# Kernel optimization log

Measured on AMD Instinct MI355X. Metric: run time of the kernel, lower is better.

## Reference

```python
import jax, jax.numpy as jnp
import numpy as np

F_, H_, W_ = 8, 24, 24          # video_shape
KS, DIL = 3, 1                  # kernel_size, dilation (cubic)
HEADS, DH, DIM = 8, 64, 512
N_TOK = F_ * H_ * W_            # 4608 video tokens (+1 BOS)
PAD = DIL * (KS - 1) // 2
SCALE = DH ** -0.5


def _geometry():
    """Precompute im2col gather indices into the padded volume and the causal mask."""
    fp, hp, wp = F_ + 2 * PAD, H_ + 2 * PAD, W_ + 2 * PAD
    tg, ig, jg = np.meshgrid(np.arange(F_), np.arange(H_), np.arange(W_), indexing='ij')
    a = np.arange(KS) * DIL
    at, ai, aj = np.meshgrid(a, a, a, indexing='ij')  # window offsets
    # query (t,i,j) in original coords == window start in padded coords
    tc = tg.reshape(-1, 1) + at.reshape(1, -1)  # [N, K3]
    ic = ig.reshape(-1, 1) + ai.reshape(1, -1)
    jc = jg.reshape(-1, 1) + aj.reshape(1, -1)
    idx = (tc * hp + ic) * wp + jc              # flat index into padded volume
    # token-id volume padded with sentinel N_TOK (matches F.pad value=max_num_tokens)
    tok = np.full((fp, hp, wp), N_TOK, dtype=np.int64)
    tok[PAD:PAD + F_, PAD:PAD + H_, PAD:PAD + W_] = np.arange(N_TOK).reshape(F_, H_, W_)
    unfolded = tok.reshape(-1)[idx]             # [N, K3]
    causal = np.arange(N_TOK)[:, None] < unfolded  # True = masked (padding is N_TOK > all)
    mask = np.concatenate([np.zeros((N_TOK, 1), bool), causal], axis=1)  # BOS never masked
    return idx, mask

_IDX_NP, _MASK_NP = _geometry()


def setup_inputs() -> dict:
    key = jax.random.key(0)
    ks = jax.random.split(key, 6)
    n = N_TOK + 1
    return {
        'x': jax.random.normal(ks[0], (1, n, DIM), jnp.float32),
        'w_q': jax.random.normal(ks[1], (DIM, HEADS * DH), jnp.float32) * 0.02,
        'w_kv': jax.random.normal(ks[2], (DIM, 2 * HEADS * DH), jnp.float32) * 0.02,
        'w_talk': jax.random.normal(ks[3], (HEADS, HEADS), jnp.float32) * 0.1,
        'w_out': jax.random.normal(ks[4], (HEADS * DH, DIM), jnp.float32) * 0.02,
        'b_out': jnp.zeros((DIM,), jnp.float32),
    }


def reference(x, w_q, w_kv, w_talk, w_out, b_out):
    idx = jnp.asarray(_IDX_NP)
    mask = jnp.asarray(_MASK_NP)
    b, n, _ = x.shape
    bh = b * HEADS
    fp, hp, wp = F_ + 2 * PAD, H_ + 2 * PAD, W_ + 2 * PAD

    q = x @ w_q                                  # [b, n, h*d]
    k, v = jnp.split(x @ w_kv, 2, axis=-1)

    def to_heads(t):
        return t.reshape(b, n, HEADS, DH).transpose(0, 2, 1, 3).reshape(bh, n, DH)

    q, k, v = map(to_heads, (q, k, v))
    q = q[:, 1:] * SCALE                         # drop BOS query
    k_bos, v_bos = k[:, :1], v[:, :1]            # [bh, 1, d]
    k, v = k[:, 1:], v[:, 1:]

    def pad_unfold(t):
        vol = t.reshape(bh, F_, H_, W_, DH)
        vol = jnp.pad(vol, ((0, 0), (PAD, PAD), (PAD, PAD), (PAD, PAD), (0, 0)))
        flat = vol.reshape(bh, fp * hp * wp, DH)
        return flat[:, idx]                      # [bh, N, K3, d]

    k_unf, v_unf = pad_unfold(k), pad_unfold(v)
    k_full = jnp.concatenate([jnp.broadcast_to(k_bos[:, None], (bh, N_TOK, 1, DH)), k_unf], axis=2)
    v_full = jnp.concatenate([jnp.broadcast_to(v_bos[:, None], (bh, N_TOK, 1, DH)), v_unf], axis=2)

    sim = jnp.einsum('bid,bijd->bij', q, k_full)           # [bh, N, 1+K3]
    sim = jnp.where(mask[None], -jnp.finfo(sim.dtype).max, sim)
    attn = jax.nn.softmax(sim, axis=-1)
    attn = attn.reshape(b, HEADS, N_TOK, -1)
    attn = jnp.einsum('gh,bhij->bgij', w_talk, attn)       # talking heads (1x1 conv)
    attn = attn.reshape(bh, N_TOK, -1)

    out = jnp.einsum('bij,bijd->bid', attn, v_full)        # [bh, N, d]
    out = jnp.concatenate([v_bos, out], axis=1)            # BOS output = v_bos
    out = out.reshape(b, HEADS, n, DH).transpose(0, 2, 1, 3).reshape(b, n, HEADS * DH)
    return out @ w_out + b_out
```

## Files before the change

### kernel.cpp

```cpp
#include <hip/hip_runtime.h>
#include <cfloat>
#include <cmath>

#define F_   8
#define H_   24
#define W_   24
#define NTOK 4608
#define NSEQ 4609
#define MPAD 4736
#define DIM  512
#define QKVC 1536
#define NNB  28
#define SCALEF 0.125f

typedef unsigned short ushort_t;
typedef __attribute__((ext_vector_type(8))) short short8v;
typedef __attribute__((ext_vector_type(8))) unsigned short ushort8v;
typedef __attribute__((ext_vector_type(4))) unsigned short ushort4v;
typedef __attribute__((ext_vector_type(4))) float floatx4;

typedef const __attribute__((address_space(1))) unsigned int guint_t;
typedef __attribute__((address_space(3))) unsigned int luint_t;

__device__ __forceinline__ float bf2f(unsigned short u) {
    return __uint_as_float(((unsigned)u) << 16);
}
__device__ __forceinline__ unsigned short f2bf(float f) {
    unsigned u = __float_as_uint(f);
    unsigned r = (u + 0x7FFFu + ((u >> 16) & 1u)) >> 16;
    return (unsigned short)r;
}

#define XBLK 1184
#define CONV_BLOCKS (XBLK + 192 + 64)

__global__ __launch_bounds__(256) void conv_k(
    const float* __restrict__ x, const float* __restrict__ wq,
    const float* __restrict__ wkv, const float* __restrict__ wout,
    ushort_t* __restrict__ xb, ushort_t* __restrict__ wcatT,
    ushort_t* __restrict__ woutT)
{
    const int bid = blockIdx.x, tid = threadIdx.x;
    __shared__ ushort_t tile[64][72];

    if (bid < XBLK) {
        int e0 = (bid * 256 + tid) * 8;
        int row = e0 >> 9;
        float4 a = make_float4(0.f, 0.f, 0.f, 0.f);
        float4 b = make_float4(0.f, 0.f, 0.f, 0.f);
        if (row < NSEQ) {
            a = *reinterpret_cast<const float4*>(&x[e0]);
            b = *reinterpret_cast<const float4*>(&x[e0 + 4]);
        }
        ushort8v o;
        o[0] = f2bf(a.x); o[1] = f2bf(a.y); o[2] = f2bf(a.z); o[3] = f2bf(a.w);
        o[4] = f2bf(b.x); o[5] = f2bf(b.y); o[6] = f2bf(b.z); o[7] = f2bf(b.w);
        *reinterpret_cast<ushort8v*>(&xb[e0]) = o;
        return;
    }

    int blk2 = bid - XBLK;
    const float* src; int ld, cb; ushort_t* dst; int k0;
    if (blk2 < 192) {
        int nt = blk2 >> 3, kt = blk2 & 7;
        int n0 = nt * 64;
        if (n0 < 512) { src = wq;  ld = 512;  cb = n0; }
        else          { src = wkv; ld = 1024; cb = n0 - 512; }
        dst = wcatT + (size_t)n0 * 512;
        k0 = kt * 64;
    } else {
        int b3 = blk2 - 192;
        int nt = b3 >> 3, kt = b3 & 7;
        src = wout; ld = 512; cb = nt * 64;
        dst = woutT + (size_t)(nt * 64) * 512;
        k0 = kt * 64;
    }

    {
        int r = tid >> 4, c4 = (tid & 15) * 4;
        #pragma unroll
        for (int p = 0; p < 4; ++p) {
            int rr = r + p * 16;
            float4 v = *reinterpret_cast<const float4*>(&src[(size_t)(k0 + rr) * ld + cb + c4]);
            tile[c4 + 0][rr] = f2bf(v.x);
            tile[c4 + 1][rr] = f2bf(v.y);
            tile[c4 + 2][rr] = f2bf(v.z);
            tile[c4 + 3][rr] = f2bf(v.w);
        }
    }
    __syncthreads();
    {
        int nl = tid >> 3, ks = (tid & 7) * 8;
        #pragma unroll
        for (int rep = 0; rep < 2; ++rep) {
            int nn = nl + rep * 32;
            ushort8v vv = *reinterpret_cast<const ushort8v*>(&tile[nn][ks]);
            *reinterpret_cast<ushort8v*>(&dst[(size_t)nn * 512 + k0 + ks]) = vv;
        }
    }
}

template<int BM, bool F32OUT>
__global__ __launch_bounds__(256, 3) void gemm_k(
    const ushort_t* __restrict__ A,
    const ushort_t* __restrict__ BT,
    const float* __restrict__ bias,
    void* __restrict__ Cv, int ldc)
{
    __shared__ ushort_t sA[BM * 64];
    __shared__ ushort_t sB[128 * 64];
    const int tid = threadIdx.x;

    const int nwg = gridDim.x * gridDim.y;
    const int orig = blockIdx.y * gridDim.x + blockIdx.x;
    const int xcd = orig & 7;
    const int qq = nwg >> 3, rr8 = nwg & 7;
    const int wg = (xcd < rr8 ? xcd * (qq + 1) : rr8 * (qq + 1) + (xcd - rr8) * qq)
                   + (orig >> 3);
    const int row0 = (wg / gridDim.x) * BM;
    const int col0 = (wg % gridDim.x) * 128;

    const int wid = tid >> 6, lane = tid & 63;
    const int wr = wid >> 1, wc = wid & 1;
    const int l15 = lane & 15, kp = lane >> 4;
    constexpr int MR = BM / 32;

    floatx4 acc[MR][4];
    #pragma unroll
    for (int m = 0; m < MR; ++m)
        #pragma unroll
        for (int n = 0; n < 4; ++n)
            acc[m][n] = (floatx4){0.f, 0.f, 0.f, 0.f};

    const ushort_t* Abase = A + (size_t)row0 * 512;
    const ushort_t* Bbase = BT + (size_t)col0 * 512;

    for (int kt = 0; kt < 8; ++kt) {
        const int k0 = kt * 64;
        #pragma unroll
        for (int rnd = 0; rnd < BM / 32; ++rnd) {
            int r = rnd * 32 + (tid >> 3);
            int gs = (tid & 7) ^ (r & 7);
            __builtin_amdgcn_global_load_lds(
                (guint_t*)(Abase + (size_t)r * 512 + k0 + gs * 8),
                (luint_t*)(sA + r * 64 + (tid & 7) * 8), 16, 0, 0);
        }
        #pragma unroll
        for (int rnd = 0; rnd < 4; ++rnd) {
            int r = rnd * 32 + (tid >> 3);
            int gs = (tid & 7) ^ (r & 7);
            __builtin_amdgcn_global_load_lds(
                (guint_t*)(Bbase + (size_t)r * 512 + k0 + gs * 8),
                (luint_t*)(sB + r * 64 + (tid & 7) * 8), 16, 0, 0);
        }
        __syncthreads();

        #pragma unroll
        for (int kk = 0; kk < 2; ++kk) {
            short8v af[MR], bfr[4];
            #pragma unroll
            for (int m = 0; m < MR; ++m) {
                int r = wr * (BM / 2) + m * 16 + l15;
                int slot = kk * 4 + kp;
                af[m] = *(const short8v*)&sA[r * 64 + ((slot ^ (r & 7)) << 3)];
            }
            #pragma unroll
            for (int n = 0; n < 4; ++n) {
                int r = wc * 64 + n * 16 + l15;
                int slot = kk * 4 + kp;
                bfr[n] = *(const short8v*)&sB[r * 64 + ((slot ^ (r & 7)) << 3)];
            }
            #pragma unroll
            for (int m = 0; m < MR; ++m)
                #pragma unroll
                for (int n = 0; n < 4; ++n)
                    acc[m][n] = __builtin_amdgcn_mfma_f32_16x16x32_bf16(
                        af[m], bfr[n], acc[m][n], 0, 0, 0);
        }
        __syncthreads();
    }

    if (!F32OUT) {
        ushort_t* C = (ushort_t*)Cv;
        #pragma unroll
        for (int m = 0; m < MR; ++m) {
            int rb = row0 + wr * (BM / 2) + m * 16 + kp * 4;
            #pragma unroll
            for (int n = 0; n < 4; ++n) {
                int col = col0 + wc * 64 + n * 16 + l15;
                #pragma unroll
                for (int q = 0; q < 4; ++q)
                    C[(size_t)(rb + q) * ldc + col] = f2bf(acc[m][n][q]);
            }
        }
    } else {
        float* C = (float*)Cv;
        #pragma unroll
        for (int m = 0; m < MR; ++m) {
            int rb = row0 + wr * (BM / 2) + m * 16 + kp * 4;
            #pragma unroll
            for (int n = 0; n < 4; ++n) {
                int col = col0 + wc * 64 + n * 16 + l15;
                float bv = bias[col];
                #pragma unroll
                for (int q = 0; q < 4; ++q)
                    if (rb + q < NSEQ)
                        C[(size_t)(rb + q) * ldc + col] = acc[m][n][q] + bv;
            }
        }
    }
}

__global__ __launch_bounds__(256) void attn_k(
    const ushort_t* __restrict__ qkv,
    const float* __restrict__ wtalk,
    ushort_t* __restrict__ outh)
{
    const int lane = threadIdx.x & 63;
    const int i = blockIdx.x * 4 + (threadIdx.x >> 6);
    const int h = lane >> 3, s = lane & 7;

    const int t = i / (H_ * W_), rem = i % (H_ * W_);
    const int yy = rem / W_, xx = rem % W_;

    int rowj = -1;
    if (lane == 0) rowj = 0;
    else if (lane < NNB) {
        int e = lane - 1;
        int dt = e / 9 - 1, dy = (e / 3) % 3 - 1, dx = e % 3 - 1;
        int nt = t + dt, ny = yy + dy, nx = xx + dx;
        bool valid = ((unsigned)nt < (unsigned)F_) && ((unsigned)ny < (unsigned)H_) &&
                     ((unsigned)nx < (unsigned)W_);
        int u = (nt * H_ + ny) * W_ + nx;
        rowj = (valid && u <= i) ? (u + 1) : -1;
    }

    int rows[NNB];
    #pragma unroll
    for (int j = 0; j < NNB; ++j) rows[j] = __shfl(rowj, j, 64);

    float qf[8];
    {
        ushort8v qv = *(const ushort8v*)&qkv[(size_t)(i + 1) * QKVC + lane * 8];
        #pragma unroll
        for (int e = 0; e < 8; ++e) qf[e] = bf2f(qv[e]);
    }

    float ps[NNB];
    #pragma unroll
    for (int j = 0; j < NNB; ++j) {
        int r = rows[j] < 0 ? 0 : rows[j];
        ushort8v kv = *(const ushort8v*)&qkv[(size_t)r * QKVC + 512 + lane * 8];
        float a = 0.f;
        #pragma unroll
        for (int e = 0; e < 8; ++e) a += qf[e] * bf2f(kv[e]);
        ps[j] = a;
    }

    float v1[14];
    {
        bool hi = (s & 1) != 0;
        #pragma unroll
        for (int m = 0; m < 14; ++m) {
            float keep = hi ? ps[2 * m + 1] : ps[2 * m];
            float oth  = hi ? ps[2 * m]     : ps[2 * m + 1];
            v1[m] = keep + __shfl_xor(oth, 1, 64);
        }
    }
    float v2[8];
    {
        bool hi = (s & 2) != 0;
        #pragma unroll
        for (int m = 0; m < 7; ++m) {
            float keep = hi ? v1[2 * m + 1] : v1[2 * m];
            float oth  = hi ? v1[2 * m]     : v1[2 * m + 1];
            v2[m] = keep + __shfl_xor(oth, 2, 64);
        }
        v2[7] = 0.f;
    }
    float simk[4];
    {
        bool hi = (s & 4) != 0;
        #pragma unroll
        for (int k = 0; k < 4; ++k) {
            float keep = hi ? v2[2 * k + 1] : v2[2 * k];
            float oth  = hi ? v2[2 * k]     : v2[2 * k + 1];
            simk[k] = keep + __shfl_xor(oth, 4, 64);
        }
    }
    #pragma unroll
    for (int k = 0; k < 4; ++k) {
        int j = s + 8 * k;
        int rj = __shfl(rowj, j, 64);
        simk[k] = (rj >= 0) ? simk[k] * SCALEF : -FLT_MAX;
    }

    float mx = fmaxf(fmaxf(simk[0], simk[1]), fmaxf(simk[2], simk[3]));
    mx = fmaxf(mx, __shfl_xor(mx, 1, 64));
    mx = fmaxf(mx, __shfl_xor(mx, 2, 64));
    mx = fmaxf(mx, __shfl_xor(mx, 4, 64));
    float att[4];
    float S = 0.f;
    #pragma unroll
    for (int k = 0; k < 4; ++k) { att[k] = __expf(simk[k] - mx); S += att[k]; }
    S += __shfl_xor(S, 1, 64);
    S += __shfl_xor(S, 2, 64);
    S += __shfl_xor(S, 4, 64);
    float inv = 1.f / S;
    #pragma unroll
    for (int k = 0; k < 4; ++k) att[k] *= inv;

    float wtg[8];
    #pragma unroll
    for (int hh = 0; hh < 8; ++hh) wtg[hh] = wtalk[h * 8 + hh];
    float pk[4];
    #pragma unroll
    for (int k = 0; k < 4; ++k) {
        float acc = 0.f;
        #pragma unroll
        for (int hh = 0; hh < 8; ++hh)
            acc += wtg[hh] * __shfl(att[k], hh * 8 + s, 64);
        pk[k] = acc;
    }

    float o[8];
    #pragma unroll
    for (int e = 0; e < 8; ++e) o[e] = 0.f;
    #pragma unroll
    for (int j = 0; j < NNB; ++j) {
        float pj = __shfl(pk[j >> 3], h * 8 + (j & 7), 64);
        int r = rows[j] < 0 ? 0 : rows[j];
        ushort8v vv = *(const ushort8v*)&qkv[(size_t)r * QKVC + 1024 + lane * 8];
        #pragma unroll
        for (int e = 0; e < 8; ++e) o[e] += pj * bf2f(vv[e]);
    }

    ushort8v ov;
    #pragma unroll
    for (int e = 0; e < 8; ++e) ov[e] = f2bf(o[e]);
    *(ushort8v*)&outh[(size_t)(i + 1) * DIM + lane * 8] = ov;

    if (i == 0) {
        ushort8v bv = *(const ushort8v*)&qkv[1024 + lane * 8];
        *(ushort8v*)&outh[lane * 8] = bv;
    }
}

extern "C" void kernel_launch(void* const* d_in, const int* in_sizes, int n_in,
                              void* d_out, int out_size, void* d_ws, size_t ws_size,
                              hipStream_t stream) {
    const float* x     = (const float*)d_in[0];
    const float* wq    = (const float*)d_in[1];
    const float* wkv   = (const float*)d_in[2];
    const float* wtalk = (const float*)d_in[3];
    const float* wout  = (const float*)d_in[4];
    const float* bout  = (const float*)d_in[5];
    float* out = (float*)d_out;

    ushort_t* xb    = (ushort_t*)d_ws;
    ushort_t* wcatT = xb    + (size_t)MPAD * 512;
    ushort_t* woutT = wcatT + (size_t)QKVC * 512;
    ushort_t* qkv   = woutT + (size_t)512 * 512;
    ushort_t* outh  = qkv   + (size_t)MPAD * QKVC;

    dim3 blk(256);
    conv_k<<<CONV_BLOCKS, blk, 0, stream>>>(x, wq, wkv, wout, xb, wcatT, woutT);
    gemm_k<128, false><<<dim3(12, 37), blk, 0, stream>>>(xb, wcatT, nullptr, qkv, QKVC);
    attn_k<<<dim3(NTOK / 4), blk, 0, stream>>>(qkv, wtalk, outh);
    gemm_k<64, true><<<dim3(4, 74), blk, 0, stream>>>(outh, woutT, bout, out, DIM);
}
```

Baseline: 53.28 us.

## Double-buffer GEMM LDS tiles and swizzle attention blocks across XCDs

The GEMM kernel now keeps two LDS buffers and issues the global-to-LDS loads for the next K tile while MFMAs run on the current one. Each iteration ends with a single waitcnt plus barrier instead of two syncs. This is meant to hide global load latency, but it doubles LDS use and lowers the occupancy hint from 3 to 2 waves per SIMD. The attention kernel also remaps block IDs so consecutive query tiles land on the same XCD, improving L2 locality for neighbour K/V rows.

```diff
diff --git a/kernel.cpp b/kernel.cpp
--- a/kernel.cpp
+++ b/kernel.cpp
@@ -16,7 +16,6 @@
 typedef unsigned short ushort_t;
 typedef __attribute__((ext_vector_type(8))) short short8v;
 typedef __attribute__((ext_vector_type(8))) unsigned short ushort8v;
-typedef __attribute__((ext_vector_type(4))) unsigned short ushort4v;
 typedef __attribute__((ext_vector_type(4))) float floatx4;
 
 typedef const __attribute__((address_space(1))) unsigned int guint_t;
@@ -101,14 +100,14 @@
 }
 
 template<int BM, bool F32OUT>
-__global__ __launch_bounds__(256, 3) void gemm_k(
+__global__ __launch_bounds__(256, 2) void gemm_k(
     const ushort_t* __restrict__ A,
     const ushort_t* __restrict__ BT,
     const float* __restrict__ bias,
     void* __restrict__ Cv, int ldc)
 {
-    __shared__ ushort_t sA[BM * 64];
-    __shared__ ushort_t sB[128 * 64];
+    __shared__ ushort_t sA[2][BM * 64];
+    __shared__ ushort_t sB[2][128 * 64];
     const int tid = threadIdx.x;
 
     const int nwg = gridDim.x * gridDim.y;
@@ -135,7 +134,7 @@
     const ushort_t* Abase = A + (size_t)row0 * 512;
     const ushort_t* Bbase = BT + (size_t)col0 * 512;
 
-    for (int kt = 0; kt < 8; ++kt) {
+    auto STAGE = [&](int buf, int kt) {
         const int k0 = kt * 64;
         #pragma unroll
         for (int rnd = 0; rnd < BM / 32; ++rnd) {
@@ -143,7 +142,7 @@
             int gs = (tid & 7) ^ (r & 7);
             __builtin_amdgcn_global_load_lds(
                 (guint_t*)(Abase + (size_t)r * 512 + k0 + gs * 8),
-                (luint_t*)(sA + r * 64 + (tid & 7) * 8), 16, 0, 0);
+                (luint_t*)(&sA[buf][r * 64 + (tid & 7) * 8]), 16, 0, 0);
         }
         #pragma unroll
         for (int rnd = 0; rnd < 4; ++rnd) {
@@ -151,10 +150,11 @@
             int gs = (tid & 7) ^ (r & 7);
             __builtin_amdgcn_global_load_lds(
                 (guint_t*)(Bbase + (size_t)r * 512 + k0 + gs * 8),
-                (luint_t*)(sB + r * 64 + (tid & 7) * 8), 16, 0, 0);
-        }
-        __syncthreads();
-
+                (luint_t*)(&sB[buf][r * 64 + (tid & 7) * 8]), 16, 0, 0);
+        }
+    };
+
+    auto COMPUTE = [&](int buf) {
         #pragma unroll
         for (int kk = 0; kk < 2; ++kk) {
             short8v af[MR], bfr[4];
@@ -162,13 +162,13 @@
             for (int m = 0; m < MR; ++m) {
                 int r = wr * (BM / 2) + m * 16 + l15;
                 int slot = kk * 4 + kp;
-                af[m] = *(const short8v*)&sA[r * 64 + ((slot ^ (r & 7)) << 3)];
+                af[m] = *(const short8v*)&sA[buf][r * 64 + ((slot ^ (r & 7)) << 3)];
             }
             #pragma unroll
             for (int n = 0; n < 4; ++n) {
                 int r = wc * 64 + n * 16 + l15;
                 int slot = kk * 4 + kp;
-                bfr[n] = *(const short8v*)&sB[r * 64 + ((slot ^ (r & 7)) << 3)];
+                bfr[n] = *(const short8v*)&sB[buf][r * 64 + ((slot ^ (r & 7)) << 3)];
             }
             #pragma unroll
             for (int m = 0; m < MR; ++m)
@@ -177,8 +177,21 @@
                     acc[m][n] = __builtin_amdgcn_mfma_f32_16x16x32_bf16(
                         af[m], bfr[n], acc[m][n], 0, 0, 0);
         }
-        __syncthreads();
-    }
+    };
+
+    STAGE(0, 0);
+    asm volatile("s_waitcnt vmcnt(0)" ::: "memory");
+    __builtin_amdgcn_s_barrier();
+    int cur = 0;
+    #pragma unroll 1
+    for (int kt = 0; kt < 7; ++kt) {
+        STAGE(cur ^ 1, kt + 1);
+        COMPUTE(cur);
+        asm volatile("s_waitcnt vmcnt(0)" ::: "memory");
+        __builtin_amdgcn_s_barrier();
+        cur ^= 1;
+    }
+    COMPUTE(cur);
 
     if (!F32OUT) {
         ushort_t* C = (ushort_t*)Cv;
@@ -217,7 +230,9 @@
     ushort_t* __restrict__ outh)
 {
     const int lane = threadIdx.x & 63;
-    const int i = blockIdx.x * 4 + (threadIdx.x >> 6);
+    const int bid0 = blockIdx.x;
+    const int bswz = (bid0 & 7) * (gridDim.x >> 3) + (bid0 >> 3);
+    const int i = bswz * 4 + (threadIdx.x >> 6);
     const int h = lane >> 3, s = lane & 7;
 
     const int t = i / (H_ * W_), rem = i % (H_ * W_);
```

New measurement: 55.89 us. 1.05x slower.
